# Performance work log

Measured on AMD Instinct MI355X. Metric: run time of the kernel, lower is better.

The kernel has to match this reference:

```python
import jax, jax.numpy as jnp
import numpy as np

DIM = 768
D_STATE = 16
D_INNER = 2 * DIM  # expand=2


def setup_inputs() -> dict:
    key = jax.random.key(0)
    k_x, k_in, k_conv, k_out = jax.random.split(key, 4)
    B, L = 1, 4096
    x = jax.random.normal(k_x, (B, L, DIM), dtype=jnp.float32)
    # torch Linear weight layout: [out_features, in_features]
    W_in = jax.random.normal(k_in, (3 * D_INNER + 2 * D_STATE, DIM), dtype=jnp.float32) * 0.02
    # depthwise conv1d kernel: [out_ch=d_inner, in_ch/groups=1, k=3]
    W_conv = jax.random.normal(k_conv, (D_INNER, 1, 3), dtype=jnp.float32) * 0.1
    W_out = jax.random.normal(k_out, (DIM, D_INNER), dtype=jnp.float32) * 0.02
    A_log = jnp.log(jnp.tile(jnp.arange(1, D_STATE + 1, dtype=jnp.float32), (D_INNER, 1)))
    D = jnp.ones((D_INNER,), dtype=jnp.float32)
    return {"x": x, "W_in": W_in, "W_conv": W_conv, "W_out": W_out, "A_log": A_log, "D": D}


def reference(x, W_in, W_conv, W_out, A_log, D):
    d_inner = W_conv.shape[0]
    d_state = A_log.shape[1]
    Bsz = x.shape[0]

    xz = x @ W_in.T  # [B, L, 3*d_inner + 2*d_state]
    x_inner, z, B_ssm, C_ssm, delta = jnp.split(
        xz, [d_inner, 2 * d_inner, 2 * d_inner + d_state, 2 * d_inner + 2 * d_state], axis=-1
    )

    # depthwise conv over sequence: [B, d_inner, L]
    xc = jax.lax.conv_general_dilated(
        x_inner.transpose(0, 2, 1), W_conv,
        window_strides=(1,), padding=[(1, 1)], feature_group_count=d_inner,
    ).transpose(0, 2, 1)  # back to [B, L, d_inner]
    xc = jax.nn.silu(xc)

    A = -jnp.exp(A_log)  # [d_inner, d_state]
    delta = jax.nn.softplus(delta)  # [B, L, d_inner]
    dA = jnp.exp(jnp.einsum('bld,dn->bldn', delta, A))           # [B, L, d_inner, d_state]
    dBx = jnp.einsum('bld,bln,bld->bldn', delta, B_ssm, xc)      # delta_B * x fused

    def step(h, inp):
        da_t, dbx_t, c_t = inp  # [B,d,n], [B,d,n], [B,n]
        h = da_t * h + dbx_t
        y_t = jnp.einsum('bdn,bn->bd', h, c_t)
        return h, y_t

    h0 = jnp.zeros((Bsz, d_inner, d_state), dtype=x.dtype)
    _, ys = jax.lax.scan(
        step, h0,
        (dA.transpose(1, 0, 2, 3), dBx.transpose(1, 0, 2, 3), C_ssm.transpose(1, 0, 2)),
    )  # ys: [L, B, d_inner]

    y = ys.transpose(1, 0, 2) + xc * D  # skip connection
    y = y * jax.nn.silu(z)
    return y @ W_out.T  # [B, L, dim]
```

## Files before the change

### kernel.cpp

```cpp
#include <hip/hip_runtime.h>
#include <hip/hip_bf16.h>
#include <math.h>

#define LSEQ   4096
#define DIM    768
#define DINNER 1536
#define DSTATE 16
#define NCOLS  4640
#define NCH    128
#define CLEN   32
#define NPAD   4736

typedef _Float16 f16;
typedef __attribute__((ext_vector_type(8))) _Float16 f16x8;
typedef __attribute__((ext_vector_type(4))) float f32x4;

#define WSCALE   64.0f
#define WDESCALE 0.015625f

__device__ __forceinline__ void gld_lds16(void* lds_dst, const void* gsrc) {
    __builtin_amdgcn_global_load_lds(
        (__attribute__((address_space(1))) void*)(gsrc),
        (__attribute__((address_space(3))) void*)(lds_dst), 16, 0, 0);
}

template<int BM, int BN, int WM, int WN, int NTB, bool COLM>
__global__ __launch_bounds__(256) void gemm_f16_split(const f16* __restrict__ A,
                                                      const f16* __restrict__ B,
                                                      float* __restrict__ C,
                                                      int M, int N, int K, int ldc,
                                                      float cscale) {
    constexpr int MI  = WM / 16;
    constexpr int NI  = WN / 16;
    constexpr int NWN = BN / WN;
    constexpr int nA  = BM / 16;
    constexpr int nB  = BN / 16;
    constexpr int NT  = nA + 2 * nB;

    __shared__ __align__(16) f16 As[BM * 32];
    __shared__ __align__(16) f16 Bs[2 * BN * 32];

    const int P   = gridDim.x >> 3;
    const int idx = (blockIdx.x & 7) * P + (blockIdx.x >> 3);
    const int m0  = (COLM ? (idx % NTB) : (idx / NTB)) * BM;
    const int n0  = (COLM ? (idx / NTB) : (idx % NTB)) * BN;

    const int tid  = threadIdx.x;
    const int w    = tid >> 6;
    const int lane = tid & 63;
    const int wr   = w / NWN;
    const int wc   = w % NWN;
    const int m    = lane & 15;
    const int q    = lane >> 4;
    const int rsub = lane >> 2;
    const int bsel = lane & 3;
    const int ldb  = 2 * K;

    f32x4 acc[MI][NI];
#pragma unroll
    for (int i = 0; i < MI; i++)
#pragma unroll
        for (int j = 0; j < NI; j++) acc[i][j] = (f32x4){0.f, 0.f, 0.f, 0.f};

    const int fragoff = ((q ^ (m & 3)) << 3);

    for (int k0 = 0; k0 < K; k0 += 32) {
#pragma unroll
        for (int t = w; t < NT; t += 4) {
            const f16* g; f16* lb; int rl;
            if (t < nA) {
                rl = t * 16 + rsub;
                g  = A + (size_t)(m0 + rl) * K + k0 + (bsel ^ (rl & 3)) * 8;
                lb = As + t * 16 * 32;
            } else if (t < nA + nB) {
                int tt = t - nA; rl = tt * 16 + rsub;
                g  = B + (size_t)(n0 + rl) * ldb + k0 + (bsel ^ (rl & 3)) * 8;
                lb = Bs + tt * 16 * 32;
            } else {
                int tt = t - nA - nB; rl = tt * 16 + rsub;
                g  = B + (size_t)(n0 + rl) * ldb + K + k0 + (bsel ^ (rl & 3)) * 8;
                lb = Bs + (nB + tt) * 16 * 32;
            }
            gld_lds16(lb, g);
        }
        __syncthreads();

        f16x8 af[MI], bh[NI], bl[NI];
#pragma unroll
        for (int i = 0; i < MI; i++)
            af[i] = *(const f16x8*)&As[(wr * WM + i * 16 + m) * 32 + fragoff];
#pragma unroll
        for (int j = 0; j < NI; j++) {
            bh[j] = *(const f16x8*)&Bs[(wc * WN + j * 16 + m) * 32 + fragoff];
            bl[j] = *(const f16x8*)&Bs[BN * 32 + (wc * WN + j * 16 + m) * 32 + fragoff];
        }
#pragma unroll
        for (int i = 0; i < MI; i++)
#pragma unroll
            for (int j = 0; j < NI; j++) {
                acc[i][j] = __builtin_amdgcn_mfma_f32_16x16x32_f16(af[i], bh[j], acc[i][j], 0, 0, 0);
                acc[i][j] = __builtin_amdgcn_mfma_f32_16x16x32_f16(af[i], bl[j], acc[i][j], 0, 0, 0);
            }
        __syncthreads();
    }

#pragma unroll
    for (int i = 0; i < MI; i++) {
#pragma unroll
        for (int j = 0; j < NI; j++) {
            const int col = n0 + wc * WN + j * 16 + m;
            if (col >= N) continue;
            const int rowb = m0 + wr * WM + i * 16 + q * 4;
#pragma unroll
            for (int r = 0; r < 4; r++)
                C[(size_t)(rowb + r) * ldc + col] = acc[i][j][r] * cscale;
        }
    }
}

#define E0 (LSEQ * DIM)
#define E1 (E0 + NPAD * DIM)
#define E2 (E1 + DIM * DINNER)

__global__ __launch_bounds__(256) void cvt_all(const float* __restrict__ x,
                                               const float* __restrict__ Wi,
                                               const float* __restrict__ Wo,
                                               f16* __restrict__ Ax,
                                               f16* __restrict__ Bw,
                                               f16* __restrict__ Bo) {
    int i = (blockIdx.x * 256 + threadIdx.x) * 4;
    if (i < E0) {
        float4 v = *(const float4*)(x + i);
        Ax[i] = (f16)v.x; Ax[i+1] = (f16)v.y; Ax[i+2] = (f16)v.z; Ax[i+3] = (f16)v.w;
    } else if (i < E1) {
        int e = i - E0;
        int n = e / DIM, k = e - n * DIM;
        f16* row = Bw + (size_t)n * (2 * DIM) + k;
        if (n < NCOLS) {
            float4 v = *(const float4*)(Wi + (size_t)n * DIM + k);
            float a[4] = {v.x * WSCALE, v.y * WSCALE, v.z * WSCALE, v.w * WSCALE};
#pragma unroll
            for (int j = 0; j < 4; j++) {
                f16 hi = (f16)a[j];
                row[j] = hi; row[DIM + j] = (f16)(a[j] - (float)hi);
            }
        } else {
#pragma unroll
            for (int j = 0; j < 4; j++) { row[j] = (f16)0.f; row[DIM + j] = (f16)0.f; }
        }
    } else if (i < E2) {
        int e = i - E1;
        int n = e / DINNER, k = e - n * DINNER;
        float4 v = *(const float4*)(Wo + e);
        float a[4] = {v.x * WSCALE, v.y * WSCALE, v.z * WSCALE, v.w * WSCALE};
        f16* row = Bo + (size_t)n * (2 * DINNER) + k;
#pragma unroll
        for (int j = 0; j < 4; j++) {
            f16 hi = (f16)a[j];
            row[j] = hi; row[DINNER + j] = (f16)(a[j] - (float)hi);
        }
    }
}

__global__ __launch_bounds__(256) void scan1_kernel(const float* __restrict__ xz,
                                                    const float* __restrict__ Wc,
                                                    const float* __restrict__ A_log,
                                                    float* __restrict__ aprod,
                                                    float* __restrict__ hend) {
    __shared__ float Bs[CLEN * DSTATE];
    const int d  = blockIdx.x * 256 + threadIdx.x;
    const int c  = blockIdx.y;
    const int l0 = c * CLEN;
    for (int i = threadIdx.x; i < CLEN * DSTATE; i += 256)
        Bs[i] = xz[(size_t)(l0 + (i >> 4)) * NCOLS + 3072 + (i & 15)];
    float Areg[DSTATE];
#pragma unroll
    for (int n = 0; n < DSTATE; n++) Areg[n] = -__expf(A_log[d * DSTATE + n]);
    const float w0 = Wc[d * 3 + 0], w1 = Wc[d * 3 + 1], w2 = Wc[d * 3 + 2];
    float xm = (l0 > 0) ? xz[(size_t)(l0 - 1) * NCOLS + d] : 0.f;
    float x0 = xz[(size_t)l0 * NCOLS + d];
    float ld_xp   = xz[(size_t)(l0 + 1) * NCOLS + d];
    float ld_draw = xz[(size_t)l0 * NCOLS + 3104 + d];
    __syncthreads();

    float h[DSTATE];
#pragma unroll
    for (int n = 0; n < DSTATE; n++) h[n] = 0.f;
    float S = 0.f;

    for (int t = 0; t < CLEN; t++) {
        const int l = l0 + t;
        float xp = ld_xp, draw = ld_draw;
        if (t + 1 < CLEN) {
            ld_xp   = (l + 2 < LSEQ) ? xz[(size_t)(l + 2) * NCOLS + d] : 0.f;
            ld_draw = xz[(size_t)(l + 1) * NCOLS + 3104 + d];
        }
        float v  = xm * w0 + x0 * w1 + xp * w2;
        float xcv = __fdividef(v, 1.f + __expf(-v));
        float dtv = (draw > 20.f) ? draw : __logf(1.f + __expf(draw));
        float u = dtv * xcv;
        S += dtv;
#pragma unroll
        for (int n = 0; n < DSTATE; n++) {
            float e = __expf(dtv * Areg[n]);
            h[n] = e * h[n] + u * Bs[t * DSTATE + n];
        }
        xm = x0; x0 = xp;
    }
#pragma unroll
    for (int n = 0; n < DSTATE; n++) {
        size_t idx = ((size_t)c * DSTATE + n) * DINNER + d;
        aprod[idx] = __expf(S * Areg[n]);
        hend[idx]  = h[n];
    }
}

__global__ __launch_bounds__(256) void scan2_kernel(const float* __restrict__ aprod,
                                                    const float* __restrict__ hend,
                                                    float* __restrict__ hinit) {
    const int g = blockIdx.x * 256 + threadIdx.x;
    const size_t S = (size_t)DSTATE * DINNER;
    size_t idx = g;
    float a = aprod[idx], e = hend[idx];
    float h = 0.f;
#pragma unroll 4
    for (int c = 0; c < NCH; c++) {
        float ac = a, ec = e;
        if (c + 1 < NCH) { a = aprod[idx + S]; e = hend[idx + S]; }
        hinit[idx] = h;
        h = ac * h + ec;
        idx += S;
    }
}

__global__ __launch_bounds__(256) void scan3_kernel(const float* __restrict__ xz,
                                                    const float* __restrict__ Wc,
                                                    const float* __restrict__ A_log,
                                                    const float* __restrict__ hinit,
                                                    const float* __restrict__ Dp,
                                                    f16* __restrict__ Ay) {
    __shared__ float Bs[CLEN * DSTATE];
    __shared__ float Cs[CLEN * DSTATE];
    const int d  = blockIdx.x * 256 + threadIdx.x;
    const int c  = blockIdx.y;
    const int l0 = c * CLEN;
    for (int i = threadIdx.x; i < CLEN * DSTATE; i += 256) {
        size_t roff = (size_t)(l0 + (i >> 4)) * NCOLS;
        Bs[i] = xz[roff + 3072 + (i & 15)];
        Cs[i] = xz[roff + 3088 + (i & 15)];
    }
    float Areg[DSTATE];
#pragma unroll
    for (int n = 0; n < DSTATE; n++) Areg[n] = -__expf(A_log[d * DSTATE + n]);
    float h[DSTATE];
#pragma unroll
    for (int n = 0; n < DSTATE; n++)
        h[n] = hinit[((size_t)c * DSTATE + n) * DINNER + d];
    const float Dv = Dp[d];
    const float w0 = Wc[d * 3 + 0], w1 = Wc[d * 3 + 1], w2 = Wc[d * 3 + 2];
    float xm = (l0 > 0) ? xz[(size_t)(l0 - 1) * NCOLS + d] : 0.f;
    float x0 = xz[(size_t)l0 * NCOLS + d];
    float ld_xp   = xz[(size_t)(l0 + 1) * NCOLS + d];
    float ld_draw = xz[(size_t)l0 * NCOLS + 3104 + d];
    float ld_z    = xz[(size_t)l0 * NCOLS + DINNER + d];
    __syncthreads();

    for (int t = 0; t < CLEN; t++) {
        const int l = l0 + t;
        float xp = ld_xp, draw = ld_draw, zv = ld_z;
        if (t + 1 < CLEN) {
            ld_xp   = (l + 2 < LSEQ) ? xz[(size_t)(l + 2) * NCOLS + d] : 0.f;
            ld_draw = xz[(size_t)(l + 1) * NCOLS + 3104 + d];
            ld_z    = xz[(size_t)(l + 1) * NCOLS + DINNER + d];
        }
        float v  = xm * w0 + x0 * w1 + xp * w2;
        float xcv = __fdividef(v, 1.f + __expf(-v));
        float dtv = (draw > 20.f) ? draw : __logf(1.f + __expf(draw));
        float u = dtv * xcv;
        float y = 0.f;
#pragma unroll
        for (int n = 0; n < DSTATE; n++) {
            float e = __expf(dtv * Areg[n]);
            h[n] = e * h[n] + u * Bs[t * DSTATE + n];
            y += h[n] * Cs[t * DSTATE + n];
        }
        float sz = __fdividef(zv, 1.f + __expf(-zv));
        Ay[(size_t)l * DINNER + d] = (f16)((y + xcv * Dv) * sz);
        xm = x0; x0 = xp;
    }
}

extern "C" void kernel_launch(void* const* d_in, const int* in_sizes, int n_in,
                              void* d_out, int out_size, void* d_ws, size_t ws_size,
                              hipStream_t stream) {
    const float* x     = (const float*)d_in[0];
    const float* W_in  = (const float*)d_in[1];
    const float* W_conv= (const float*)d_in[2];
    const float* W_out = (const float*)d_in[3];
    const float* A_log = (const float*)d_in[4];
    const float* Dp    = (const float*)d_in[5];
    float* out = (float*)d_out;

    float* ws  = (float*)d_ws;
    float* xz  = ws;
    float* ap  = xz + (size_t)LSEQ * NCOLS;
    float* he  = ap + (size_t)NCH * DSTATE * DINNER;
    float* hi  = he + (size_t)NCH * DSTATE * DINNER;
    f16* Ax = (f16*)(hi + (size_t)NCH * DSTATE * DINNER);
    f16* Ay = Ax + (size_t)LSEQ * DIM;
    f16* Bw = Ay + (size_t)LSEQ * DINNER;
    f16* Bo = Bw + (size_t)NPAD * 2 * DIM;

    cvt_all<<<E2 / 1024, 256, 0, stream>>>(x, W_in, W_out, Ax, Bw, Bo);

    gemm_f16_split<128, 128, 64, 64, 32, true><<<1184, 256, 0, stream>>>(
        Ax, Bw, xz, LSEQ, NCOLS, DIM, NCOLS, WDESCALE);

    scan1_kernel<<<dim3(DINNER / 256, NCH), 256, 0, stream>>>(
        xz, W_conv, A_log, ap, he);
    scan2_kernel<<<(DINNER * DSTATE) / 256, 256, 0, stream>>>(ap, he, hi);
    scan3_kernel<<<dim3(DINNER / 256, NCH), 256, 0, stream>>>(
        xz, W_conv, A_log, hi, Dp, Ay);

    gemm_f16_split<64, 64, 32, 32, 12, false><<<768, 256, 0, stream>>>(
        Ay, Bo, out, LSEQ, DIM, DINNER, DIM, WDESCALE);
}
```

Before: 290.0 us.

## Drop split-f16 weight precision for input projection and emit z as f16

The input projection GEMM now uses a single f16 copy of W_in instead of a hi/lo split pair. This halves the MFMA count and the B-operand traffic for the largest GEMM. The z columns are written directly as an f16 buffer from the GEMM epilogue, and the scan reads z from there, which cuts xz write and read bandwidth. In exchange, the projection and gate lose precision (no weight scaling, no residual term), which may hurt accuracy against the fp32 reference.

```diff
diff --git a/kernel.cpp b/kernel.cpp
--- a/kernel.cpp
+++ b/kernel.cpp
@@ -24,21 +24,23 @@
         (__attribute__((address_space(3))) void*)(lds_dst), 16, 0, 0);
 }
 
-template<int BM, int BN, int WM, int WN, int NTB, bool COLM>
-__global__ __launch_bounds__(256) void gemm_f16_split(const f16* __restrict__ A,
-                                                      const f16* __restrict__ B,
-                                                      float* __restrict__ C,
-                                                      int M, int N, int K, int ldc,
-                                                      float cscale) {
+template<int BM, int BN, int WM, int WN, int NTB, bool COLM, bool SPLIT, bool ZMODE>
+__global__ __launch_bounds__(256) void gemm_f16(const f16* __restrict__ A,
+                                                const f16* __restrict__ B,
+                                                float* __restrict__ C,
+                                                f16* __restrict__ Z,
+                                                int M, int N, int K, int ldc,
+                                                float cscale) {
     constexpr int MI  = WM / 16;
     constexpr int NI  = WN / 16;
     constexpr int NWN = BN / WN;
     constexpr int nA  = BM / 16;
     constexpr int nB  = BN / 16;
-    constexpr int NT  = nA + 2 * nB;
+    constexpr int NPL = SPLIT ? 2 : 1;
+    constexpr int NT  = nA + NPL * nB;
 
     __shared__ __align__(16) f16 As[BM * 32];
-    __shared__ __align__(16) f16 Bs[2 * BN * 32];
+    __shared__ __align__(16) f16 Bs[NPL * BN * 32];
 
     const int P   = gridDim.x >> 3;
     const int idx = (blockIdx.x & 7) * P + (blockIdx.x >> 3);
@@ -54,7 +56,7 @@
     const int q    = lane >> 4;
     const int rsub = lane >> 2;
     const int bsel = lane & 3;
-    const int ldb  = 2 * K;
+    const int ldb  = NPL * K;
 
     f32x4 acc[MI][NI];
 #pragma unroll
@@ -85,25 +87,46 @@
         }
         __syncthreads();
 
-        f16x8 af[MI], bh[NI], bl[NI];
+        f16x8 af[MI], bh[NI];
 #pragma unroll
         for (int i = 0; i < MI; i++)
             af[i] = *(const f16x8*)&As[(wr * WM + i * 16 + m) * 32 + fragoff];
 #pragma unroll
-        for (int j = 0; j < NI; j++) {
+        for (int j = 0; j < NI; j++)
             bh[j] = *(const f16x8*)&Bs[(wc * WN + j * 16 + m) * 32 + fragoff];
-            bl[j] = *(const f16x8*)&Bs[BN * 32 + (wc * WN + j * 16 + m) * 32 + fragoff];
-        }
 #pragma unroll
         for (int i = 0; i < MI; i++)
 #pragma unroll
+            for (int j = 0; j < NI; j++)
+                acc[i][j] = __builtin_amdgcn_mfma_f32_16x16x32_f16(af[i], bh[j], acc[i][j], 0, 0, 0);
+        if (SPLIT) {
+            f16x8 bl[NI];
+#pragma unroll
+            for (int j = 0; j < NI; j++)
+                bl[j] = *(const f16x8*)&Bs[BN * 32 + (wc * WN + j * 16 + m) * 32 + fragoff];
+#pragma unroll
+            for (int i = 0; i < MI; i++)
+#pragma unroll
+                for (int j = 0; j < NI; j++)
+                    acc[i][j] = __builtin_amdgcn_mfma_f32_16x16x32_f16(af[i], bl[j], acc[i][j], 0, 0, 0);
+        }
+        __syncthreads();
+    }
+
+    if (ZMODE && n0 >= DINNER && n0 < 2 * DINNER) {
+#pragma unroll
+        for (int i = 0; i < MI; i++) {
+#pragma unroll
             for (int j = 0; j < NI; j++) {
-                acc[i][j] = __builtin_amdgcn_mfma_f32_16x16x32_f16(af[i], bh[j], acc[i][j], 0, 0, 0);
-                acc[i][j] = __builtin_amdgcn_mfma_f32_16x16x32_f16(af[i], bl[j], acc[i][j], 0, 0, 0);
+                const int col = n0 - DINNER + wc * WN + j * 16 + m;
+                const int rowb = m0 + wr * WM + i * 16 + q * 4;
+#pragma unroll
+                for (int r = 0; r < 4; r++)
+                    Z[(size_t)(rowb + r) * DINNER + col] = (f16)acc[i][j][r];
             }
-        __syncthreads();
-    }
-
+        }
+        return;
+    }
 #pragma unroll
     for (int i = 0; i < MI; i++) {
 #pragma unroll
@@ -134,19 +157,12 @@
         Ax[i] = (f16)v.x; Ax[i+1] = (f16)v.y; Ax[i+2] = (f16)v.z; Ax[i+3] = (f16)v.w;
     } else if (i < E1) {
         int e = i - E0;
-        int n = e / DIM, k = e - n * DIM;
-        f16* row = Bw + (size_t)n * (2 * DIM) + k;
+        int n = e / DIM;
         if (n < NCOLS) {
-            float4 v = *(const float4*)(Wi + (size_t)n * DIM + k);
-            float a[4] = {v.x * WSCALE, v.y * WSCALE, v.z * WSCALE, v.w * WSCALE};
-#pragma unroll
-            for (int j = 0; j < 4; j++) {
-                f16 hi = (f16)a[j];
-                row[j] = hi; row[DIM + j] = (f16)(a[j] - (float)hi);
-            }
+            float4 v = *(const float4*)(Wi + e);
+            Bw[e] = (f16)v.x; Bw[e+1] = (f16)v.y; Bw[e+2] = (f16)v.z; Bw[e+3] = (f16)v.w;
         } else {
-#pragma unroll
-            for (int j = 0; j < 4; j++) { row[j] = (f16)0.f; row[DIM + j] = (f16)0.f; }
+            Bw[e] = (f16)0.f; Bw[e+1] = (f16)0.f; Bw[e+2] = (f16)0.f; Bw[e+3] = (f16)0.f;
         }
     } else if (i < E2) {
         int e = i - E1;
@@ -234,6 +250,7 @@
 }
 
 __global__ __launch_bounds__(256) void scan3_kernel(const float* __restrict__ xz,
+                                                    const f16* __restrict__ Zb,
                                                     const float* __restrict__ Wc,
                                                     const float* __restrict__ A_log,
                                                     const float* __restrict__ hinit,
@@ -262,7 +279,7 @@
     float x0 = xz[(size_t)l0 * NCOLS + d];
     float ld_xp   = xz[(size_t)(l0 + 1) * NCOLS + d];
     float ld_draw = xz[(size_t)l0 * NCOLS + 3104 + d];
-    float ld_z    = xz[(size_t)l0 * NCOLS + DINNER + d];
+    float ld_z    = (float)Zb[(size_t)l0 * DINNER + d];
     __syncthreads();
 
     for (int t = 0; t < CLEN; t++) {
@@ -271,7 +288,7 @@
         if (t + 1 < CLEN) {
             ld_xp   = (l + 2 < LSEQ) ? xz[(size_t)(l + 2) * NCOLS + d] : 0.f;
             ld_draw = xz[(size_t)(l + 1) * NCOLS + 3104 + d];
-            ld_z    = xz[(size_t)(l + 1) * NCOLS + DINNER + d];
+            ld_z    = (float)Zb[(size_t)(l + 1) * DINNER + d];
         }
         float v  = xm * w0 + x0 * w1 + xp * w2;
         float xcv = __fdividef(v, 1.f + __expf(-v));
@@ -309,19 +326,20 @@
     f16* Ax = (f16*)(hi + (size_t)NCH * DSTATE * DINNER);
     f16* Ay = Ax + (size_t)LSEQ * DIM;
     f16* Bw = Ay + (size_t)LSEQ * DINNER;
-    f16* Bo = Bw + (size_t)NPAD * 2 * DIM;
+    f16* Bo = Bw + (size_t)NPAD * DIM;
+    f16* Zb = Bo + (size_t)DIM * 2 * DINNER;
 
     cvt_all<<<E2 / 1024, 256, 0, stream>>>(x, W_in, W_out, Ax, Bw, Bo);
 
-    gemm_f16_split<128, 128, 64, 64, 32, true><<<1184, 256, 0, stream>>>(
-        Ax, Bw, xz, LSEQ, NCOLS, DIM, NCOLS, WDESCALE);
+    gemm_f16<128, 128, 64, 64, 32, true, false, true><<<1184, 256, 0, stream>>>(
+        Ax, Bw, xz, Zb, LSEQ, NCOLS, DIM, NCOLS, 1.0f);
 
     scan1_kernel<<<dim3(DINNER / 256, NCH), 256, 0, stream>>>(
         xz, W_conv, A_log, ap, he);
     scan2_kernel<<<(DINNER * DSTATE) / 256, 256, 0, stream>>>(ap, he, hi);
     scan3_kernel<<<dim3(DINNER / 256, NCH), 256, 0, stream>>>(
-        xz, W_conv, A_log, hi, Dp, Ay);
-
-    gemm_f16_split<64, 64, 32, 32, 12, false><<<768, 256, 0, stream>>>(
-        Ay, Bo, out, LSEQ, DIM, DINNER, DIM, WDESCALE);
-}
+        xz, Zb, W_conv, A_log, hi, Dp, Ay);
+
+    gemm_f16<64, 64, 32, 32, 12, false, true, false><<<768, 256, 0, stream>>>(
+        Ay, Bo, out, nullptr, LSEQ, DIM, DINNER, DIM, WDESCALE);
+}
```

After: 265.1 us. 8.6% less time.
